# Kernel tuning notes

Measured on AMD Instinct MI355X. Metric: run time of the kernel, lower is better.

## Reference

```python
import jax, jax.numpy as jnp
import numpy as np

N_NODES = 50000
N_EDGES = 1200000
IN_SIZE = 128
HID = 64
OUT = 64
NEG_SLOPE = 0.01  # torch F.leaky_relu default


def setup_inputs() -> dict:
    key = jax.random.key(0)
    ks = jax.random.split(key, 8)
    x = jax.random.normal(ks[0], (N_NODES, IN_SIZE), dtype=jnp.float32)
    edge_weight = jax.random.uniform(ks[1], (N_EDGES,), dtype=jnp.float32)
    W1 = jax.random.normal(ks[2], (IN_SIZE, HID), dtype=jnp.float32) / np.sqrt(IN_SIZE)
    b1 = jax.random.normal(ks[3], (HID,), dtype=jnp.float32) * 0.01
    W2 = jax.random.normal(ks[4], (HID, OUT), dtype=jnp.float32) / np.sqrt(HID)
    b2 = jax.random.normal(ks[5], (OUT,), dtype=jnp.float32) * 0.01
    src = jax.random.randint(ks[6], (N_EDGES,), 0, N_NODES, dtype=jnp.int64 if jax.config.jax_enable_x64 else jnp.int32)
    dst = jax.random.randint(ks[7], (N_EDGES,), 0, N_NODES, dtype=jnp.int64 if jax.config.jax_enable_x64 else jnp.int32)
    return {"x": x, "edge_weight": edge_weight, "W1": W1, "b1": b1,
            "W2": W2, "b2": b2, "src": src, "dst": dst}


def _wg_layer(h, W, b, src, dst, edge_weight, n_nodes):
    # Linear projection on all nodes: [N, d_out]
    Wh = h @ W + b
    # u_mul_e: gather source features, scale by scalar edge weight -> [E, d_out]
    msg = Wh[src] * edge_weight[:, None]
    # fn.mean('m','h'): segment-mean by destination node
    s = jax.ops.segment_sum(msg, dst, num_segments=n_nodes)
    deg = jax.ops.segment_sum(jnp.ones_like(edge_weight), dst, num_segments=n_nodes)
    return s / jnp.maximum(deg, 1.0)[:, None]  # isolated nodes -> 0 (DGL default)


def reference(x, edge_weight, W1, b1, W2, b2, src, dst):
    n = x.shape[0]
    h1 = _wg_layer(x, W1, b1, src, dst, edge_weight, n)
    h1 = jax.nn.leaky_relu(h1, negative_slope=NEG_SLOPE)
    out = _wg_layer(h1, W2, b2, src, dst, edge_weight, n)
    return out
```

## Files before the change

### kernel.cpp

```cpp
#include <hip/hip_runtime.h>
#include <hip/hip_fp16.h>


#define N_NODES 50000
#define N_EDGES 1200000
#define IN_SIZE 128
#define HID 64
#define NEG_SLOPE 0.01f
#define NBB 391
#define SLOTC 3456
#define FILL_EPB 8192
#define FILL_BLOCKS ((N_EDGES + FILL_EPB - 1) / FILL_EPB)
#define GEMM_BLOCKS ((N_NODES + 255) / 256)
#define RS2 (HID + 8)

typedef _Float16 half8 __attribute__((ext_vector_type(8)));
typedef float floatx4 __attribute__((ext_vector_type(4)));

template <int K>
__device__ __forceinline__ void gemm_body(int blk,
                                          const float* __restrict__ A,
                                          const float* __restrict__ W,
                                          const float* __restrict__ b,
                                          _Float16* __restrict__ out,
                                          _Float16* wthi, _Float16* wtlo) {
    constexpr int RS = K + 8;
    const int tid = threadIdx.x;
    for (int i = tid; i < 64 * K; i += 1024) {
        int n = i / K, k = i % K;
        float wv = W[k * 64 + n];
        _Float16 hi = (_Float16)wv;
        wthi[n * RS + k] = hi;
        wtlo[n * RS + k] = (_Float16)(wv - (float)hi);
    }
    __syncthreads();

    const int lane = tid & 63;
    const int wid = tid >> 6;
    const int q = lane >> 4, c = lane & 15;

    int arow = blk * 256 + wid * 16 + c;
    int lrow = min(arow, N_NODES - 1);
    const float* ap = A + (size_t)lrow * K + q * 8;

    floatx4 acc0 = {b[c],      b[c],      b[c],      b[c]};
    floatx4 acc1 = {b[c + 16], b[c + 16], b[c + 16], b[c + 16]};
    floatx4 acc2 = {b[c + 32], b[c + 32], b[c + 32], b[c + 32]};
    floatx4 acc3 = {b[c + 48], b[c + 48], b[c + 48], b[c + 48]};

#pragma unroll
    for (int ks = 0; ks < K / 32; ++ks) {
        float4 f0 = ((const float4*)(ap + ks * 32))[0];
        float4 f1 = ((const float4*)(ap + ks * 32))[1];
        float fv[8] = {f0.x, f0.y, f0.z, f0.w, f1.x, f1.y, f1.z, f1.w};
        half8 ahi, alo;
#pragma unroll
        for (int j = 0; j < 8; ++j) {
            _Float16 h = (_Float16)fv[j];
            ahi[j] = h;
            alo[j] = (_Float16)(fv[j] - (float)h);
        }
        const int kb = ks * 32 + q * 8;
        half8 bh0 = *(const half8*)&wthi[(c     ) * RS + kb];
        half8 bl0 = *(const half8*)&wtlo[(c     ) * RS + kb];
        half8 bh1 = *(const half8*)&wthi[(c + 16) * RS + kb];
        half8 bl1 = *(const half8*)&wtlo[(c + 16) * RS + kb];
        half8 bh2 = *(const half8*)&wthi[(c + 32) * RS + kb];
        half8 bl2 = *(const half8*)&wtlo[(c + 32) * RS + kb];
        half8 bh3 = *(const half8*)&wthi[(c + 48) * RS + kb];
        half8 bl3 = *(const half8*)&wtlo[(c + 48) * RS + kb];
        acc0 = __builtin_amdgcn_mfma_f32_16x16x32_f16(ahi, bh0, acc0, 0, 0, 0);
        acc0 = __builtin_amdgcn_mfma_f32_16x16x32_f16(ahi, bl0, acc0, 0, 0, 0);
        acc0 = __builtin_amdgcn_mfma_f32_16x16x32_f16(alo, bh0, acc0, 0, 0, 0);
        acc1 = __builtin_amdgcn_mfma_f32_16x16x32_f16(ahi, bh1, acc1, 0, 0, 0);
        acc1 = __builtin_amdgcn_mfma_f32_16x16x32_f16(ahi, bl1, acc1, 0, 0, 0);
        acc1 = __builtin_amdgcn_mfma_f32_16x16x32_f16(alo, bh1, acc1, 0, 0, 0);
        acc2 = __builtin_amdgcn_mfma_f32_16x16x32_f16(ahi, bh2, acc2, 0, 0, 0);
        acc2 = __builtin_amdgcn_mfma_f32_16x16x32_f16(ahi, bl2, acc2, 0, 0, 0);
        acc2 = __builtin_amdgcn_mfma_f32_16x16x32_f16(alo, bh2, acc2, 0, 0, 0);
        acc3 = __builtin_amdgcn_mfma_f32_16x16x32_f16(ahi, bh3, acc3, 0, 0, 0);
        acc3 = __builtin_amdgcn_mfma_f32_16x16x32_f16(ahi, bl3, acc3, 0, 0, 0);
        acc3 = __builtin_amdgcn_mfma_f32_16x16x32_f16(alo, bh3, acc3, 0, 0, 0);
    }

    int rowb = blk * 256 + wid * 16 + q * 4;
#pragma unroll
    for (int r = 0; r < 4; ++r) {
        if (rowb + r < N_NODES) {
            _Float16* op = out + (size_t)(rowb + r) * HID + c;
            op[0]  = (_Float16)acc0[r];
            op[16] = (_Float16)acc1[r];
            op[32] = (_Float16)acc2[r];
            op[48] = (_Float16)acc3[r];
        }
    }
}

__device__ __forceinline__ void fill_body(int blk,
                                          const int* __restrict__ src,
                                          const int* __restrict__ dst,
                                          const float* __restrict__ ew,
                                          int* __restrict__ gcur,
                                          int2* __restrict__ epack,
                                          int* lhist, int* lbase) {
    const int tid = threadIdx.x;
    const int e0 = blk * FILL_EPB;
    if (tid < NBB) lhist[tid] = 0;

    const int g0 = e0 + 4 * tid, g1 = g0 + 4096;
    const bool a0 = g0 < N_EDGES, a1 = g1 < N_EDGES;
    int4 d0 = {0,0,0,0}, d1 = {0,0,0,0}, s0 = {0,0,0,0}, s1 = {0,0,0,0};
    float4 w0 = {0,0,0,0}, w1 = {0,0,0,0};
    if (a0) { d0 = *(const int4*)(dst + g0); s0 = *(const int4*)(src + g0);
              w0 = *(const float4*)(ew + g0); }
    if (a1) { d1 = *(const int4*)(dst + g1); s1 = *(const int4*)(src + g1);
              w1 = *(const float4*)(ew + g1); }
    __syncthreads();

    if (a0) { atomicAdd(&lhist[d0.x >> 7], 1); atomicAdd(&lhist[d0.y >> 7], 1);
              atomicAdd(&lhist[d0.z >> 7], 1); atomicAdd(&lhist[d0.w >> 7], 1); }
    if (a1) { atomicAdd(&lhist[d1.x >> 7], 1); atomicAdd(&lhist[d1.y >> 7], 1);
              atomicAdd(&lhist[d1.z >> 7], 1); atomicAdd(&lhist[d1.w >> 7], 1); }
    __syncthreads();

    if (tid < NBB) {
        int c = lhist[tid];
        lbase[tid] = tid * SLOTC + (c ? atomicAdd(&gcur[tid], c) : 0);
        lhist[tid] = 0;
    }
    __syncthreads();

    const int dd0[4] = {d0.x, d0.y, d0.z, d0.w};
    const int ss0[4] = {s0.x, s0.y, s0.z, s0.w};
    const float ww0[4] = {w0.x, w0.y, w0.z, w0.w};
    const int dd1[4] = {d1.x, d1.y, d1.z, d1.w};
    const int ss1[4] = {s1.x, s1.y, s1.z, s1.w};
    const float ww1[4] = {w1.x, w1.y, w1.z, w1.w};
    if (a0) {
#pragma unroll
        for (int j = 0; j < 4; ++j) {
            int d = dd0[j], b = d >> 7;
            int idx = lbase[b] + atomicAdd(&lhist[b], 1);
            if (idx < (b + 1) * SLOTC)
                epack[idx] = make_int2(ss0[j] | ((d & 127) << 16),
                                       __float_as_int(ww0[j]));
        }
    }
    if (a1) {
#pragma unroll
        for (int j = 0; j < 4; ++j) {
            int d = dd1[j], b = d >> 7;
            int idx = lbase[b] + atomicAdd(&lhist[b], 1);
            if (idx < (b + 1) * SLOTC)
                epack[idx] = make_int2(ss1[j] | ((d & 127) << 16),
                                       __float_as_int(ww1[j]));
        }
    }
}

__global__ __launch_bounds__(1024) void fill_gemm1(const int* __restrict__ src,
                                                   const int* __restrict__ dst,
                                                   const float* __restrict__ ew,
                                                   int* __restrict__ gcur,
                                                   int2* __restrict__ epack,
                                                   const float* __restrict__ x,
                                                   const float* __restrict__ W1,
                                                   const float* __restrict__ b1,
                                                   _Float16* __restrict__ outA) {
    __shared__ union SU {
        struct { int lhist[NBB]; int lbase[NBB]; } f;
        struct { _Float16 hi[64 * (IN_SIZE + 8)];
                 _Float16 lo[64 * (IN_SIZE + 8)]; } g;
    } u;
    if (blockIdx.x < FILL_BLOCKS)
        fill_body(blockIdx.x, src, dst, ew, gcur, epack,
                  u.f.lhist, u.f.lbase);
    else
        gemm_body<IN_SIZE>(blockIdx.x - FILL_BLOCKS, x, W1, b1, outA,
                           u.g.hi, u.g.lo);
}

__global__ __launch_bounds__(1024) void sort_agg1_gemm2(
        const int* __restrict__ gcur,
        const int2* __restrict__ epack,
        const _Float16* __restrict__ Wh1,
        const float* __restrict__ W2, const float* __restrict__ b2,
        unsigned int* __restrict__ esort, int* __restrict__ off,
        _Float16* __restrict__ outB) {
    __shared__ unsigned int lsort[SLOTC];
    __shared__ int cnt[128];
    __shared__ int start[128];
    __shared__ int wsum[2];
    __shared__ _Float16 w2hi[64 * RS2];
    __shared__ _Float16 w2lo[64 * RS2];
    __shared__ union AU {
        struct { unsigned int pay[SLOTC]; unsigned char d7[SLOTC]; } s;
        _Float16 hs[128 * RS2];
    } u;
    const int tid = threadIdx.x;
    const int bkt = blockIdx.x;
    const int beg = bkt * SLOTC;
    const int n = min(gcur[bkt], SLOTC);

    for (int i = tid; i < 64 * HID; i += 1024) {
        int nn = i >> 6, k = i & 63;
        float wv = W2[k * 64 + nn];
        _Float16 hi = (_Float16)wv;
        w2hi[nn * RS2 + k] = hi;
        w2lo[nn * RS2 + k] = (_Float16)(wv - (float)hi);
    }
    if (tid < 128) cnt[tid] = 0;
    __syncthreads();

    for (int e = tid; e < n; e += 1024) {
        int2 pk = epack[beg + e];
        int d7 = (pk.x >> 16) & 127;
        unsigned short hw = __half_as_ushort(__float2half(__int_as_float(pk.y)));
        u.s.pay[e] = (unsigned int)(pk.x & 0xffff) | ((unsigned int)hw << 16);
        u.s.d7[e] = (unsigned char)d7;
        atomicAdd(&cnt[d7], 1);
    }
    __syncthreads();

    int orig = 0, incl = 0;
    if (tid < 128) {
        orig = cnt[tid];
        int v = orig;
        for (int o = 1; o < 64; o <<= 1) {
            int t = __shfl_up(v, o);
            if ((tid & 63) >= o) v += t;
        }
        if ((tid & 63) == 63) wsum[tid >> 6] = v;
        incl = v;
    }
    __syncthreads();
    if (tid < 128) {
        if (tid >= 64) incl += wsum[0];
        int excl = incl - orig;
        start[tid] = excl;
        off[bkt * 129 + tid] = beg + excl;
        if (tid == 127) off[bkt * 129 + 128] = beg + incl;
        cnt[tid] = 0;
    }
    __syncthreads();

    for (int e = tid; e < n; e += 1024) {
        int d7 = u.s.d7[e];
        int pos = atomicAdd(&cnt[d7], 1);
        int idx = start[d7] + pos;
        if (idx < SLOTC)
            lsort[idx] = u.s.pay[e];
    }
    __syncthreads();

    for (int i = tid; i < n; i += 1024)
        esort[beg + i] = lsort[i];

    {
        const int lane = tid & 63;
        const int g = lane >> 3, p = lane & 7;
        const int nl = (tid >> 6) * 8 + g;
        const int lbeg = start[nl];
        const int deg = cnt[nl];
        float acc[8] = {0, 0, 0, 0, 0, 0, 0, 0};
        const int lend = min(lbeg + deg, SLOTC);
        for (int e = lbeg; e < lend; ++e) {
            const unsigned int pe = lsort[e];
            const float w =
                __half2float(__ushort_as_half((unsigned short)(pe >> 16)));
            half8 row = *(const half8*)(Wh1 + (size_t)(pe & 0xffff) * HID + p * 8);
#pragma unroll
            for (int j = 0; j < 8; ++j)
                acc[j] = fmaf((float)row[j], w, acc[j]);
        }
        const float inv = 1.0f / fmaxf((float)deg, 1.0f);
        half8 hv;
#pragma unroll
        for (int j = 0; j < 8; ++j) {
            float t = acc[j] * inv;
            t = t >= 0.0f ? t : NEG_SLOPE * t;
            hv[j] = (_Float16)t;
        }
        *(half8*)&u.hs[nl * RS2 + p * 8] = hv;
    }
    __syncthreads();

    {
        const int lane = tid & 63, wid = tid >> 6;
        const int q = lane >> 4, c = lane & 15;
        const int r = wid >> 1, ch = wid & 1;
        floatx4 acc0 = {b2[ch * 32 + c], b2[ch * 32 + c],
                        b2[ch * 32 + c], b2[ch * 32 + c]};
        floatx4 acc1 = {b2[ch * 32 + 16 + c], b2[ch * 32 + 16 + c],
                        b2[ch * 32 + 16 + c], b2[ch * 32 + 16 + c]};
#pragma unroll
        for (int ks = 0; ks < 2; ++ks) {
            const int kb = ks * 32 + q * 8;
            half8 a = *(const half8*)&u.hs[(r * 16 + c) * RS2 + kb];
            half8 bh0 = *(const half8*)&w2hi[(ch * 32 + c) * RS2 + kb];
            half8 bl0 = *(const half8*)&w2lo[(ch * 32 + c) * RS2 + kb];
            half8 bh1 = *(const half8*)&w2hi[(ch * 32 + 16 + c) * RS2 + kb];
            half8 bl1 = *(const half8*)&w2lo[(ch * 32 + 16 + c) * RS2 + kb];
            acc0 = __builtin_amdgcn_mfma_f32_16x16x32_f16(a, bh0, acc0, 0, 0, 0);
            acc0 = __builtin_amdgcn_mfma_f32_16x16x32_f16(a, bl0, acc0, 0, 0, 0);
            acc1 = __builtin_amdgcn_mfma_f32_16x16x32_f16(a, bh1, acc1, 0, 0, 0);
            acc1 = __builtin_amdgcn_mfma_f32_16x16x32_f16(a, bl1, acc1, 0, 0, 0);
        }
        const int rowb = bkt * 128 + r * 16 + q * 4;
#pragma unroll
        for (int rr = 0; rr < 4; ++rr) {
            if (rowb + rr < N_NODES) {
                _Float16* op = outB + (size_t)(rowb + rr) * HID + ch * 32 + c;
                op[0]  = (_Float16)acc0[rr];
                op[16] = (_Float16)acc1[rr];
            }
        }
    }
}

__global__ __launch_bounds__(256) void agg2_k(const _Float16* __restrict__ Wh,
                                              const int* __restrict__ off,
                                              const unsigned int* __restrict__ es,
                                              float* __restrict__ out) {
    const int tid = threadIdx.x;
    const int lane = tid & 63;
    const int wid = tid >> 6;
    const int g = lane >> 3, p = lane & 7;
    const int node = blockIdx.x * 32 + wid * 8 + g;
    const bool valid = node < N_NODES;
    int beg = 0, end = 0;
    if (valid) {
        const int o = (node >> 7) * 129 + (node & 127);
        beg = off[o];
        end = off[o + 1];
    }
    const int deg = end - beg;

    unsigned int pld[5];
#pragma unroll
    for (int c = 0; c < 5; ++c) {
        int e = beg + c * 8 + p;
        pld[c] = (e < end) ? es[e] : 0u;
    }

    int mdeg = deg;
#pragma unroll
    for (int mask = 8; mask <= 32; mask <<= 1)
        mdeg = max(mdeg, __shfl_xor(mdeg, mask));

    float acc[8] = {0, 0, 0, 0, 0, 0, 0, 0};
#pragma unroll
    for (int c = 0; c < 5; ++c) {
        if (c * 8 >= mdeg) break;
#pragma unroll
        for (int s = 0; s < 8; ++s) {
            const unsigned int pe = __shfl(pld[c], (g << 3) | s);
            const bool act = beg + c * 8 + s < end;
            const int srow = act ? (int)(pe & 0xffff) : 0;
            const float w = act
                ? __half2float(__ushort_as_half((unsigned short)(pe >> 16)))
                : 0.0f;
            half8 row = *(const half8*)(Wh + (size_t)srow * HID + p * 8);
#pragma unroll
            for (int j = 0; j < 8; ++j)
                acc[j] = fmaf((float)row[j], w, acc[j]);
        }
    }
    for (int e = beg + 40; e < end; ++e) {
        const unsigned int pe = es[e];
        const float w =
            __half2float(__ushort_as_half((unsigned short)(pe >> 16)));
        half8 row = *(const half8*)(Wh + (size_t)(pe & 0xffff) * HID + p * 8);
#pragma unroll
        for (int j = 0; j < 8; ++j)
            acc[j] = fmaf((float)row[j], w, acc[j]);
    }

    if (valid) {
        const float inv = 1.0f / fmaxf((float)deg, 1.0f);
        float4* op = (float4*)(out + (size_t)node * HID + p * 8);
        op[0] = make_float4(acc[0] * inv, acc[1] * inv, acc[2] * inv, acc[3] * inv);
        op[1] = make_float4(acc[4] * inv, acc[5] * inv, acc[6] * inv, acc[7] * inv);
    }
}

extern "C" void kernel_launch(void* const* d_in, const int* in_sizes, int n_in,
                              void* d_out, int out_size, void* d_ws, size_t ws_size,
                              hipStream_t stream) {
    const float* x  = (const float*)d_in[0];
    const float* ew = (const float*)d_in[1];
    const float* W1 = (const float*)d_in[2];
    const float* b1 = (const float*)d_in[3];
    const float* W2 = (const float*)d_in[4];
    const float* b2 = (const float*)d_in[5];
    const int* src  = (const int*)d_in[6];
    const int* dst  = (const int*)d_in[7];
    float* out = (float*)d_out;

    const int NH = N_NODES * HID;
    const int ES = NBB * SLOTC;

    int* gcur = (int*)d_ws;
    int* off  = gcur + 400;
    unsigned int* esort = (unsigned int*)(off + 50448);
    int2* epack = (int2*)(esort + ES);
    _Float16* bufA = (_Float16*)(epack + ES);
    _Float16* bufB = bufA + NH;

    const int agg2Blocks = (N_NODES + 31) / 32;

    hipMemsetAsync(gcur, 0, 400 * sizeof(int), stream);

    fill_gemm1<<<FILL_BLOCKS + GEMM_BLOCKS, 1024, 0, stream>>>(
        src, dst, ew, gcur, epack, x, W1, b1, bufA);

    sort_agg1_gemm2<<<NBB, 1024, 0, stream>>>(
        gcur, epack, bufA, W2, b2, esort, off, bufB);

    agg2_k<<<agg2Blocks, 256, 0, stream>>>(bufB, off, esort, out);
}
```

Before: 76.90 us.

## Stage fill scatter in LDS for coalesced writes and compact edge payload

```diff
diff --git a/kernel.cpp b/kernel.cpp
--- a/kernel.cpp
+++ b/kernel.cpp
@@ -96,16 +96,27 @@
     }
 }
 
+struct FillLds {
+    unsigned int spay[FILL_EPB];
+    unsigned short saux[FILL_EPB];
+    int lhist[NBB];
+    int lbase[NBB];
+    int lstart[NBB];
+    int wsum[8];
+};
+
 __device__ __forceinline__ void fill_body(int blk,
                                           const int* __restrict__ src,
                                           const int* __restrict__ dst,
                                           const float* __restrict__ ew,
                                           int* __restrict__ gcur,
-                                          int2* __restrict__ epack,
-                                          int* lhist, int* lbase) {
+                                          unsigned int* __restrict__ epay,
+                                          unsigned char* __restrict__ ed7,
+                                          FillLds& f) {
     const int tid = threadIdx.x;
     const int e0 = blk * FILL_EPB;
-    if (tid < NBB) lhist[tid] = 0;
+    const int nblk = min(FILL_EPB, N_EDGES - e0);
+    if (tid < NBB) f.lhist[tid] = 0;
 
     const int g0 = e0 + 4 * tid, g1 = g0 + 4096;
     const bool a0 = g0 < N_EDGES, a1 = g1 < N_EDGES;
@@ -117,16 +128,32 @@
               w1 = *(const float4*)(ew + g1); }
     __syncthreads();
 
-    if (a0) { atomicAdd(&lhist[d0.x >> 7], 1); atomicAdd(&lhist[d0.y >> 7], 1);
-              atomicAdd(&lhist[d0.z >> 7], 1); atomicAdd(&lhist[d0.w >> 7], 1); }
-    if (a1) { atomicAdd(&lhist[d1.x >> 7], 1); atomicAdd(&lhist[d1.y >> 7], 1);
-              atomicAdd(&lhist[d1.z >> 7], 1); atomicAdd(&lhist[d1.w >> 7], 1); }
-    __syncthreads();
-
+    if (a0) { atomicAdd(&f.lhist[d0.x >> 7], 1); atomicAdd(&f.lhist[d0.y >> 7], 1);
+              atomicAdd(&f.lhist[d0.z >> 7], 1); atomicAdd(&f.lhist[d0.w >> 7], 1); }
+    if (a1) { atomicAdd(&f.lhist[d1.x >> 7], 1); atomicAdd(&f.lhist[d1.y >> 7], 1);
+              atomicAdd(&f.lhist[d1.z >> 7], 1); atomicAdd(&f.lhist[d1.w >> 7], 1); }
+    __syncthreads();
+
+    int orig = 0, v = 0;
     if (tid < NBB) {
-        int c = lhist[tid];
-        lbase[tid] = tid * SLOTC + (c ? atomicAdd(&gcur[tid], c) : 0);
-        lhist[tid] = 0;
+        orig = f.lhist[tid];
+        v = orig;
+        for (int o = 1; o < 64; o <<= 1) {
+            int t = __shfl_up(v, o);
+            if ((tid & 63) >= o) v += t;
+        }
+        if ((tid & 63) == 63 || tid == NBB - 1) f.wsum[tid >> 6] = v;
+    }
+    __syncthreads();
+    if (tid < NBB) {
+        int w = tid >> 6;
+        int incl = v;
+        for (int k = 0; k < w; ++k) incl += f.wsum[k];
+        int excl = incl - orig;
+        f.lstart[tid] = excl;
+        int gb = orig ? atomicAdd(&gcur[tid], orig) : 0;
+        f.lbase[tid] = tid * SLOTC + gb - excl;
+        f.lhist[tid] = 0;
     }
     __syncthreads();
 
@@ -140,20 +167,31 @@
 #pragma unroll
         for (int j = 0; j < 4; ++j) {
             int d = dd0[j], b = d >> 7;
-            int idx = lbase[b] + atomicAdd(&lhist[b], 1);
-            if (idx < (b + 1) * SLOTC)
-                epack[idx] = make_int2(ss0[j] | ((d & 127) << 16),
-                                       __float_as_int(ww0[j]));
+            unsigned short hw = __half_as_ushort(__float2half(ww0[j]));
+            int pos = f.lstart[b] + atomicAdd(&f.lhist[b], 1);
+            f.spay[pos] = (unsigned int)(ss0[j] & 0xffff) | ((unsigned int)hw << 16);
+            f.saux[pos] = (unsigned short)((d & 127) | (b << 7));
         }
     }
     if (a1) {
 #pragma unroll
         for (int j = 0; j < 4; ++j) {
             int d = dd1[j], b = d >> 7;
-            int idx = lbase[b] + atomicAdd(&lhist[b], 1);
-            if (idx < (b + 1) * SLOTC)
-                epack[idx] = make_int2(ss1[j] | ((d & 127) << 16),
-                                       __float_as_int(ww1[j]));
+            unsigned short hw = __half_as_ushort(__float2half(ww1[j]));
+            int pos = f.lstart[b] + atomicAdd(&f.lhist[b], 1);
+            f.spay[pos] = (unsigned int)(ss1[j] & 0xffff) | ((unsigned int)hw << 16);
+            f.saux[pos] = (unsigned short)((d & 127) | (b << 7));
+        }
+    }
+    __syncthreads();
+
+    for (int i = tid; i < nblk; i += 1024) {
+        int aux = f.saux[i];
+        int b = aux >> 7;
+        int gi = f.lbase[b] + i;
+        if (gi < (b + 1) * SLOTC) {
+            epay[gi] = f.spay[i];
+            ed7[gi] = (unsigned char)(aux & 127);
         }
     }
 }
@@ -162,19 +200,19 @@
                                                    const int* __restrict__ dst,
                                                    const float* __restrict__ ew,
                                                    int* __restrict__ gcur,
-                                                   int2* __restrict__ epack,
+                                                   unsigned int* __restrict__ epay,
+                                                   unsigned char* __restrict__ ed7,
                                                    const float* __restrict__ x,
                                                    const float* __restrict__ W1,
                                                    const float* __restrict__ b1,
                                                    _Float16* __restrict__ outA) {
     __shared__ union SU {
-        struct { int lhist[NBB]; int lbase[NBB]; } f;
+        FillLds f;
         struct { _Float16 hi[64 * (IN_SIZE + 8)];
                  _Float16 lo[64 * (IN_SIZE + 8)]; } g;
     } u;
     if (blockIdx.x < FILL_BLOCKS)
-        fill_body(blockIdx.x, src, dst, ew, gcur, epack,
-                  u.f.lhist, u.f.lbase);
+        fill_body(blockIdx.x, src, dst, ew, gcur, epay, ed7, u.f);
     else
         gemm_body<IN_SIZE>(blockIdx.x - FILL_BLOCKS, x, W1, b1, outA,
                            u.g.hi, u.g.lo);
@@ -182,7 +220,8 @@
 
 __global__ __launch_bounds__(1024) void sort_agg1_gemm2(
         const int* __restrict__ gcur,
-        const int2* __restrict__ epack,
+        const unsigned int* __restrict__ epay,
+        const unsigned char* __restrict__ ed7,
         const _Float16* __restrict__ Wh1,
         const float* __restrict__ W2, const float* __restrict__ b2,
         unsigned int* __restrict__ esort, int* __restrict__ off,
@@ -213,10 +252,8 @@
     __syncthreads();
 
     for (int e = tid; e < n; e += 1024) {
-        int2 pk = epack[beg + e];
-        int d7 = (pk.x >> 16) & 127;
-        unsigned short hw = __half_as_ushort(__float2half(__int_as_float(pk.y)));
-        u.s.pay[e] = (unsigned int)(pk.x & 0xffff) | ((unsigned int)hw << 16);
+        int d7 = ed7[beg + e];
+        u.s.pay[e] = epay[beg + e];
         u.s.d7[e] = (unsigned char)d7;
         atomicAdd(&cnt[d7], 1);
     }
@@ -403,8 +440,9 @@
     int* gcur = (int*)d_ws;
     int* off  = gcur + 400;
     unsigned int* esort = (unsigned int*)(off + 50448);
-    int2* epack = (int2*)(esort + ES);
-    _Float16* bufA = (_Float16*)(epack + ES);
+    unsigned int* epay = esort + ES;
+    unsigned char* ed7 = (unsigned char*)(epay + ES);
+    _Float16* bufA = (_Float16*)(ed7 + ES);
     _Float16* bufB = bufA + NH;
 
     const int agg2Blocks = (N_NODES + 31) / 32;
@@ -412,10 +450,10 @@
     hipMemsetAsync(gcur, 0, 400 * sizeof(int), stream);
 
     fill_gemm1<<<FILL_BLOCKS + GEMM_BLOCKS, 1024, 0, stream>>>(
-        src, dst, ew, gcur, epack, x, W1, b1, bufA);
+        src, dst, ew, gcur, epay, ed7, x, W1, b1, bufA);
 
     sort_agg1_gemm2<<<NBB, 1024, 0, stream>>>(
-        gcur, epack, bufA, W2, b2, esort, off, bufB);
+        gcur, epay, ed7, bufA, W2, b2, esort, off, bufB);
 
     agg2_k<<<agg2Blocks, 256, 0, stream>>>(bufB, off, esort, out);
 }
```

Measured after the change: 74.30 us (median of 2 runs). 1.04x faster.
